# Performance work log

Measured on AMD Instinct MI355X. Metric: run time of the kernel, lower is better.

The kernel has to match this reference:

```python
import jax, jax.numpy as jnp
import numpy as np

NUM_HEADS = 8
CODEBOOK_SIZE = 1024
HEAD_DIM = 128
BATCH = 32768


def setup_inputs() -> dict:
    key = jax.random.key(0)
    k_z, k_cb = jax.random.split(key)
    z = jax.random.normal(k_z, (BATCH, NUM_HEADS * HEAD_DIM), dtype=jnp.float32)
    codebooks = jax.random.normal(k_cb, (NUM_HEADS, CODEBOOK_SIZE, HEAD_DIM), dtype=jnp.float32)
    return {"z": z, "codebooks": codebooks}


def reference(z, codebooks):
    # z: [B, H*D]; codebooks: [H, K, D]
    H, K, D = codebooks.shape
    B = z.shape[0]
    zh = z.reshape(B, H, D)
    # Squared euclidean distances ||z - c||^2 = ||z||^2 - 2 z.c + ||c||^2.
    # torch.cdist(p=2) applies sqrt, but sqrt is monotone so argmin is identical.
    z_sq = jnp.sum(zh * zh, axis=-1)                       # [B, H]
    c_sq = jnp.sum(codebooks * codebooks, axis=-1)         # [H, K]
    cross = jnp.einsum('bhd,hkd->bhk', zh, codebooks)      # [B, H, K]
    d2 = z_sq[:, :, None] - 2.0 * cross + c_sq[None, :, :]  # [B, H, K]
    idx = jnp.argmin(d2, axis=-1)                          # [B, H] int
    # Gather nearest codes per head: codebooks[h, idx[b,h]] -> [B, H, D]
    zq = codebooks[jnp.arange(H)[None, :], idx]
    # Straight-through estimator: forward = codes, backward = identity on z.
    zq = zh + jax.lax.stop_gradient(zq - zh)
    return zq.reshape(B, H * D), idx
```

## Files before the change

kernel.cpp:

```cpp
#include <hip/hip_runtime.h>

namespace {
constexpr int kNH = 8;
constexpr int kK  = 1024;
constexpr int kD  = 128;
constexpr int kB  = 32768;

constexpr int BM  = 128;
constexpr int kMarginQ = 4;
constexpr float kMarginF32 = 0.0625f;

constexpr size_t kOffCsq = 4096;
constexpr size_t kOffCbF = 65536;
constexpr size_t kOffWl  = 65536 + 2 * 2097152;
}

typedef short bf16x8 __attribute__((ext_vector_type(8)));
typedef float f32x16 __attribute__((ext_vector_type(16)));

__device__ __forceinline__ unsigned short f2bf_rne(float f) {
    unsigned int x = __float_as_uint(f);
    unsigned int r = (x + 0x7fffu + ((x >> 16) & 1u)) >> 16;
    return (unsigned short)r;
}
__device__ __forceinline__ float bf2f(unsigned short u) {
    return __uint_as_float(((unsigned int)u) << 16);
}

__global__ void pq_prep(const float* __restrict__ cb,
                        unsigned short* __restrict__ cbf,
                        float* __restrict__ csq)
{
    int code = blockIdx.x;
    int t = threadIdx.x;
    int h = code >> 10, k = code & 1023;
    int kt = k >> 6, cv = (k >> 5) & 1, l31 = k & 31;
    int kc = t >> 4, hh = (t >> 3) & 1, j = t & 7;
    float v = cb[(size_t)code * kD + t];
    unsigned short hb = f2bf_rne(v);
    unsigned short lb = f2bf_rne(v - bf2f(hb));
    size_t base = ((((size_t)h * 16 + kt) * 8 + kc) * 2 + cv) * 2048;
    size_t off  = base + (hh * 32 + l31) * 16 + j * 2;
    *(unsigned short*)((char*)cbf + off)        = hb;
    *(unsigned short*)((char*)cbf + off + 1024) = lb;
    __shared__ double red[128];
    red[t] = (double)v * (double)v;
    __syncthreads();
    for (int s = 64; s > 0; s >>= 1) {
        if (t < s) red[t] += red[t + s];
        __syncthreads();
    }
    if (t == 0) csq[code] = (float)(red[0] * 1024.0);
}

__global__ __launch_bounds__(256, 2)
void pq_coarse_mfma3(const float* __restrict__ z, const float* __restrict__ cb,
                     const unsigned short* __restrict__ cbf,
                     const float* __restrict__ csq1024,
                     float* __restrict__ out_zq, float* __restrict__ out_idx,
                     unsigned int* wl_count, unsigned int* wl, unsigned int wl_cap)
{
    __shared__ float csq_s[kK];
    __shared__ int   idx_s[BM];

    const int t    = threadIdx.x;
    const int h    = blockIdx.y;
    const int b0   = blockIdx.x * BM;
    const int lane = t & 63;
    const int w    = t >> 6;
    const int l31  = lane & 31, h32 = lane >> 5;

    *(float4*)&csq_s[t * 4] = *(const float4*)(csq1024 + h * kK + t * 4);

    bf16x8 Ah[8], Al[8];
    {
        const float* zr = z + (size_t)(b0 + w * 32 + l31) * (kNH * kD) + h * kD + h32 * 8;
        #pragma unroll
        for (int kc = 0; kc < 8; ++kc) {
            float4 a = *(const float4*)(zr + kc * 16);
            float4 b = *(const float4*)(zr + kc * 16 + 4);
            float f[8] = {a.x, a.y, a.z, a.w, b.x, b.y, b.z, b.w};
            bf16x8 hv, lv;
            #pragma unroll
            for (int j = 0; j < 8; ++j) {
                unsigned short hb = f2bf_rne(f[j]);
                hv[j] = (short)hb;
                lv[j] = (short)f2bf_rne(f[j] - bf2f(hb));
            }
            Ah[kc] = hv;
            Al[kc] = lv;
        }
    }
    __syncthreads();

    int b1[16], b2[16];
    #pragma unroll
    for (int r = 0; r < 16; ++r) { b1[r] = 0x7fffffff; b2[r] = 0x7fffffff; }

    const char* bbase = (const char*)cbf + (size_t)h * 524288 + lane * 16;
#define LDSLOT(kt_, kc_, s_)                                                  \
    {                                                                         \
        const char* p_ = bbase + (size_t)(((kt_) * 8 + (kc_)) * 2) * 2048;    \
        Bh0[s_] = *(const bf16x8*)(p_);                                       \
        Bl0[s_] = *(const bf16x8*)(p_ + 1024);                                \
        Bh1[s_] = *(const bf16x8*)(p_ + 2048);                                \
        Bl1[s_] = *(const bf16x8*)(p_ + 3072);                                \
    }

    bf16x8 Bh0[4], Bl0[4], Bh1[4], Bl1[4];
    LDSLOT(0, 0, 0);
    LDSLOT(0, 1, 1);

    for (int kt = 0; kt < 16; ++kt) {
        f32x16 acc0 = (f32x16)0.0f, acc1 = (f32x16)0.0f;
        const int ktn = (kt + 1 < 16) ? kt + 1 : kt;
        #pragma unroll
        for (int kc = 0; kc < 8; ++kc) {
            const int s  = kc & 3;
            const int s2 = (kc + 2) & 3;
            if (kc < 6) {
                LDSLOT(kt, kc + 2, s2);
            } else {
                LDSLOT(ktn, kc - 6, s2);
            }
            __builtin_amdgcn_s_setprio(1);
            acc0 = __builtin_amdgcn_mfma_f32_32x32x16_bf16(Ah[kc], Bh0[s], acc0, 0, 0, 0);
            acc1 = __builtin_amdgcn_mfma_f32_32x32x16_bf16(Ah[kc], Bh1[s], acc1, 0, 0, 0);
            acc0 = __builtin_amdgcn_mfma_f32_32x32x16_bf16(Al[kc], Bh0[s], acc0, 0, 0, 0);
            acc1 = __builtin_amdgcn_mfma_f32_32x32x16_bf16(Al[kc], Bh1[s], acc1, 0, 0, 0);
            acc0 = __builtin_amdgcn_mfma_f32_32x32x16_bf16(Ah[kc], Bl0[s], acc0, 0, 0, 0);
            acc1 = __builtin_amdgcn_mfma_f32_32x32x16_bf16(Ah[kc], Bl1[s], acc1, 0, 0, 0);
            __builtin_amdgcn_s_setprio(0);
        }
        const float cs0 = csq_s[kt * 64 + l31];
        const float cs1 = csq_s[kt * 64 + 32 + l31];
        const int   kg0 = kt * 64 + l31, kg1 = kg0 + 32;
        #pragma unroll
        for (int r = 0; r < 16; ++r) {
            {
                float kf = fmaf(acc0[r], -2048.0f, cs0);
                int key = ((int)kf << 10) + kg0;
                int mx = max(b1[r], key);
                b1[r] = min(b1[r], key);
                b2[r] = min(b2[r], mx);
            }
            {
                float kf = fmaf(acc1[r], -2048.0f, cs1);
                int key = ((int)kf << 10) + kg1;
                int mx = max(b1[r], key);
                b1[r] = min(b1[r], key);
                b2[r] = min(b2[r], mx);
            }
        }
    }
#undef LDSLOT

    #pragma unroll
    for (int r = 0; r < 16; ++r) {
        int v1 = b1[r], v2 = b2[r];
        #pragma unroll
        for (int m = 1; m < 32; m <<= 1) {
            int o1 = __shfl_xor(v1, m);
            int o2 = __shfl_xor(v2, m);
            int mx = max(v1, o1);
            v1 = min(v1, o1);
            v2 = min(min(v2, o2), mx);
        }
        if (l31 == 0) {
            int row = w * 32 + (r & 3) + ((r >> 2) << 3) + h32 * 4;
            int idx = v1 & 1023;
            idx_s[row] = idx;
            int gid = (b0 + row) * kNH + h;
            out_idx[gid] = (float)idx;
            if (wl_cap > 0u && ((v2 >> 10) - (v1 >> 10)) <= kMarginQ) {
                unsigned int pos = atomicAdd(wl_count, 1u);
                if (pos < wl_cap) wl[pos] = (unsigned int)gid;
            }
        }
    }
    __syncthreads();
    {
        const float* cbh_row = cb + (size_t)h * kK * kD;
        #pragma unroll
        for (int it = 0; it < 16; ++it) {
            int c = it * 256 + t;
            int row = c >> 5, col4 = c & 31;
            *(float4*)(out_zq + (size_t)(b0 + row) * (kNH * kD) + h * kD + col4 * 4) =
                *(const float4*)(cbh_row + (size_t)idx_s[row] * kD + col4 * 4);
        }
    }
}

__global__ __launch_bounds__(256, 2)
void pq_coarse_f32(const float* __restrict__ z, const float* __restrict__ cb,
                   float* __restrict__ out_zq, float* __restrict__ out_idx,
                   unsigned int* wl_count, unsigned int* wl, unsigned int wl_cap)
{
    constexpr int KT = 64, PAD = 68, BMF = 64;
    __shared__ float zT[kD][PAD];
    __shared__ float cT[kD][PAD];
    __shared__ float csq_s[KT];
    __shared__ int   bidx_s[BMF];

    const int t  = threadIdx.x;
    const int h  = blockIdx.y;
    const int b0 = blockIdx.x * BMF;
    const int tx = t & 15, ty = t >> 4;
    const int r8 = t & 7,  d4 = t >> 3;

    {
        const float* zp = z + (size_t)(b0 + r8) * (kNH * kD) + h * kD + 4 * d4;
        #pragma unroll
        for (int it = 0; it < BMF / 8; ++it) {
            float4 v = *(const float4*)(zp + (size_t)(8 * it) * (kNH * kD));
            int r = r8 + 8 * it;
            zT[4 * d4 + 0][r] = v.x; zT[4 * d4 + 1][r] = v.y;
            zT[4 * d4 + 2][r] = v.z; zT[4 * d4 + 3][r] = v.w;
        }
    }
    float best1[4], best2[4]; int ibest[4];
    #pragma unroll
    for (int i = 0; i < 4; ++i) { best1[i] = 3.4e38f; best2[i] = 3.4e38f; ibest[i] = 0; }

    for (int kt = 0; kt < kK / KT; ++kt) {
        __syncthreads();
        {
            const float* cp = cb + ((size_t)h * kK + kt * KT + r8) * kD + 4 * d4;
            #pragma unroll
            for (int it = 0; it < KT / 8; ++it) {
                float4 v = *(const float4*)(cp + (size_t)(8 * it) * kD);
                int r = r8 + 8 * it;
                cT[4 * d4 + 0][r] = v.x; cT[4 * d4 + 1][r] = v.y;
                cT[4 * d4 + 2][r] = v.z; cT[4 * d4 + 3][r] = v.w;
            }
        }
        if (t < KT) csq_s[t] = 0.0f;
        __syncthreads();
        {
            int kk = t & 63, part = t >> 6;
            float s = 0.f;
            #pragma unroll
            for (int i = 0; i < 32; ++i) { float v = cT[32 * part + i][kk]; s = fmaf(v, v, s); }
            atomicAdd(&csq_s[kk], s);
        }
        __syncthreads();
        float accA[4][4] = {{0}}, accB[4][4] = {{0}};
        #pragma unroll 2
        for (int d = 0; d < kD; d += 2) {
            float4 za = *(const float4*)&zT[d][4 * ty];
            float4 ca = *(const float4*)&cT[d][4 * tx];
            float4 zb = *(const float4*)&zT[d + 1][4 * ty];
            float4 cv = *(const float4*)&cT[d + 1][4 * tx];
            float zav[4] = {za.x, za.y, za.z, za.w}, cav[4] = {ca.x, ca.y, ca.z, ca.w};
            float zbv[4] = {zb.x, zb.y, zb.z, zb.w}, cbv[4] = {cv.x, cv.y, cv.z, cv.w};
            #pragma unroll
            for (int i = 0; i < 4; ++i)
                #pragma unroll
                for (int j = 0; j < 4; ++j) {
                    accA[i][j] = fmaf(zav[i], cav[j], accA[i][j]);
                    accB[i][j] = fmaf(zbv[i], cbv[j], accB[i][j]);
                }
        }
        #pragma unroll
        for (int j = 0; j < 4; ++j) {
            int kk = 4 * tx + j;
            float cs = csq_s[kk];
            int kg = kt * KT + kk;
            #pragma unroll
            for (int i = 0; i < 4; ++i) {
                float s = fmaf(-2.0f, accA[i][j] + accB[i][j], cs);
                if (s < best1[i]) { best2[i] = best1[i]; best1[i] = s; ibest[i] = kg; }
                else if (s < best2[i]) { best2[i] = s; }
            }
        }
    }
    __syncthreads();
    float* redv1 = &zT[0][0];
    float* redv2 = redv1 + BMF * 16;
    int*   redi  = (int*)(redv2 + BMF * 16);
    #pragma unroll
    for (int i = 0; i < 4; ++i) {
        int r = 4 * ty + i;
        redv1[r * 16 + tx] = best1[i]; redv2[r * 16 + tx] = best2[i]; redi[r * 16 + tx] = ibest[i];
    }
    __syncthreads();
    if (t < BMF) {
        int r = t;
        float vb1_ = redv1[r * 16], vb2_ = redv2[r * 16];
        int i1 = redi[r * 16];
        #pragma unroll
        for (int x = 1; x < 16; ++x) {
            float nb1 = redv1[r * 16 + x], nb2 = redv2[r * 16 + x];
            int ni1 = redi[r * 16 + x];
            if (nb1 < vb1_ || (nb1 == vb1_ && ni1 < i1)) { vb2_ = fminf(vb1_, nb2); vb1_ = nb1; i1 = ni1; }
            else vb2_ = fminf(vb2_, nb1);
        }
        bidx_s[r] = i1;
        int gid = (b0 + r) * kNH + h;
        out_idx[gid] = (float)i1;
        if (wl_cap > 0u && (vb2_ - vb1_) <= kMarginF32) {
            unsigned int pos = atomicAdd(wl_count, 1u);
            if (pos < wl_cap) wl[pos] = (unsigned int)gid;
        }
    }
    __syncthreads();
    {
        int r = t >> 2, q = t & 3;
        const float* src = cb + ((size_t)h * kK + bidx_s[r]) * kD;
        float* dst = out_zq + (size_t)(b0 + r) * (kNH * kD) + h * kD;
        #pragma unroll
        for (int m = 0; m < 8; ++m) {
            int jj = 4 * m + q;
            *(float4*)(dst + 4 * jj) = *(const float4*)(src + 4 * jj);
        }
    }
}

__global__ __launch_bounds__(256)
void pq_exact(const float* __restrict__ z, const float* __restrict__ cb,
              float* __restrict__ out_zq, float* __restrict__ out_idx,
              const unsigned int* wl_count, const unsigned int* wl,
              unsigned int wl_cap)
{
    if (wl_cap == 0u) return;
    __shared__ float  zs[kD];
    __shared__ double rv[256];
    __shared__ int    ri[256];
    unsigned int n = *wl_count;
    if (n > wl_cap) n = wl_cap;
    const int t = threadIdx.x;
    for (unsigned int e = blockIdx.x; e < n; e += gridDim.x) {
        unsigned int id = wl[e];
        int b = (int)(id / kNH), h = (int)(id % kNH);
        if (t < kD) zs[t] = z[(size_t)b * (kNH * kD) + h * kD + t];
        __syncthreads();
        double bv = 1e300; int bi = 0;
        #pragma unroll
        for (int kk = 0; kk < 4; ++kk) {
            int k = t * 4 + kk;
            const float* c = cb + ((size_t)h * kK + k) * kD;
            double s = 0.0;
            for (int d = 0; d < kD; ++d) {
                double diff = (double)zs[d] - (double)c[d];
                s = fma(diff, diff, s);
            }
            if (s < bv) { bv = s; bi = k; }
        }
        rv[t] = bv; ri[t] = bi;
        __syncthreads();
        for (int s2 = 128; s2 > 0; s2 >>= 1) {
            if (t < s2) {
                if (rv[t + s2] < rv[t] || (rv[t + s2] == rv[t] && ri[t + s2] < ri[t])) {
                    rv[t] = rv[t + s2]; ri[t] = ri[t + s2];
                }
            }
            __syncthreads();
        }
        int kbest = ri[0];
        if (t == 0) out_idx[id] = (float)kbest;
        if (t < kD)
            out_zq[(size_t)b * (kNH * kD) + h * kD + t] =
                cb[((size_t)h * kK + kbest) * kD + t];
        __syncthreads();
    }
}

extern "C" void kernel_launch(void* const* d_in, const int* in_sizes, int n_in,
                              void* d_out, int out_size, void* d_ws, size_t ws_size,
                              hipStream_t stream)
{
    const float* z  = (const float*)d_in[0];
    const float* cb = (const float*)d_in[1];
    float* out_zq  = (float*)d_out;
    float* out_idx = out_zq + (size_t)kB * kNH * kD;
    char* ws = (char*)d_ws;

    if (ws_size >= kOffWl + 4096) {
        unsigned int* wl_count = (unsigned int*)ws;
        unsigned int* wl = (unsigned int*)(ws + kOffWl);
        size_t c = (ws_size - kOffWl) / 4;
        unsigned int cap = (unsigned int)(c > 262144 ? 262144 : c);
        float* csq = (float*)(ws + kOffCsq);
        unsigned short* cbf = (unsigned short*)(ws + kOffCbF);

        hipMemsetAsync(d_ws, 0, 4, stream);
        pq_prep<<<kNH * kK, kD, 0, stream>>>(cb, cbf, csq);
        dim3 grid(kB / BM, kNH);
        pq_coarse_mfma3<<<grid, 256, 0, stream>>>(z, cb, cbf, csq,
                                                  out_zq, out_idx, wl_count, wl, cap);
        pq_exact<<<256, 256, 0, stream>>>(z, cb, out_zq, out_idx, wl_count, wl, cap);
    } else {
        unsigned int* wl_count = (unsigned int*)ws;
        unsigned int* wl = wl_count + 1;
        unsigned int cap = 0;
        if (ws_size >= 64) {
            size_t c = ws_size / 4 - 1;
            cap = (unsigned int)(c > 262144 ? 262144 : c);
            hipMemsetAsync(d_ws, 0, 4, stream);
        }
        dim3 grid(kB / 64, kNH);
        pq_coarse_f32<<<grid, 256, 0, stream>>>(z, cb, out_zq, out_idx, wl_count, wl, cap);
        pq_exact<<<256, 256, 0, stream>>>(z, cb, out_zq, out_idx, wl_count, wl, cap);
    }
}
```

Measured before the change: 252.9 us.

## Keep codebook slices in registers and stream z tiles through LDS

Adds a new coarse kernel that keeps each wave's 64-code slice of the split-bf16 codebook resident in registers. It streams 32-row tiles of z through double-buffered, swizzled LDS, converting z to hi/lo bf16 on the fly. Work is split across two codebook halves. Each block writes per-row top-2 partial keys to a workspace, and a new merge kernel combines the halves, writes indices and gathered codes, and builds the refinement worklist. This trades the old per-block codebook streaming for codebook reuse across many z rows. The cost is an extra kernel launch, a partial-result buffer round trip, and a larger workspace requirement that falls back to the old path when unavailable.

Measured after the change: 238.4 us. 5.7% less time.

```diff
diff --git a/kernel.cpp b/kernel.cpp
--- a/kernel.cpp
+++ b/kernel.cpp
@@ -10,13 +10,16 @@
 constexpr int kMarginQ = 4;
 constexpr float kMarginF32 = 0.0625f;
 
-constexpr size_t kOffCsq = 4096;
-constexpr size_t kOffCbF = 65536;
-constexpr size_t kOffWl  = 65536 + 2 * 2097152;
-}
-
-typedef short bf16x8 __attribute__((ext_vector_type(8)));
-typedef float f32x16 __attribute__((ext_vector_type(16)));
+constexpr size_t kOffCsq  = 4096;
+constexpr size_t kOffCbF  = 65536;
+constexpr size_t kOffPart = 65536 + 4194304;
+constexpr size_t kOffWl6  = 65536 + 8388608;
+constexpr size_t kOffWl5  = 65536 + 4194304;
+}
+
+typedef short           bf16x8 __attribute__((ext_vector_type(8)));
+typedef unsigned short  us16x8 __attribute__((ext_vector_type(8)));
+typedef float           f32x16 __attribute__((ext_vector_type(16)));
 
 __device__ __forceinline__ unsigned short f2bf_rne(float f) {
     unsigned int x = __float_as_uint(f);
@@ -53,6 +56,173 @@
     if (t == 0) csq[code] = (float)(red[0] * 1024.0);
 }
 
+__global__ __launch_bounds__(512, 2)
+void pq_coarse_mfma4(const float* __restrict__ z,
+                     const unsigned short* __restrict__ cbf,
+                     const float* __restrict__ csq1024,
+                     int2* __restrict__ part)
+{
+    __shared__ unsigned short zbuf[2][2][32 * kD];
+    __shared__ int2 P[2][8][32];
+
+    const int t    = threadIdx.x;
+    const int lane = t & 63;
+    const int w    = t >> 6;
+    const int l31  = lane & 31, h32 = lane >> 5;
+    const int h    = blockIdx.y;
+    const int half = blockIdx.z;
+    const int rb0  = blockIdx.x * 1024;
+
+    bf16x8 Ah[8][2], Al[8][2];
+    {
+        const char* base = (const char*)cbf
+            + (((size_t)h * 16 + half * 8 + w) * 16) * 2048 + lane * 16;
+        #pragma unroll
+        for (int kc = 0; kc < 8; ++kc)
+            #pragma unroll
+            for (int cv = 0; cv < 2; ++cv) {
+                const char* p = base + (size_t)(kc * 2 + cv) * 2048;
+                Ah[kc][cv] = *(const bf16x8*)p;
+                Al[kc][cv] = *(const bf16x8*)(p + 1024);
+            }
+    }
+    float csel[2][16];
+    {
+        const float* cs = csq1024 + h * kK + half * 512 + w * 64 + h32 * 4;
+        #pragma unroll
+        for (int cv = 0; cv < 2; ++cv)
+            #pragma unroll
+            for (int r = 0; r < 16; ++r)
+                csel[cv][r] = cs[cv * 32 + (r & 3) + ((r >> 2) << 3)];
+    }
+
+    float4 zA, zB;
+    auto issueZ = [&](int tile) {
+        const float* zp = z + (size_t)(rb0 + tile * 32 + (t >> 4)) * (kNH * kD)
+                            + h * kD + (t & 15) * 8;
+        zA = *(const float4*)zp;
+        zB = *(const float4*)(zp + 4);
+    };
+    auto commitZ = [&](int buf) {
+        float f[8] = {zA.x, zA.y, zA.z, zA.w, zB.x, zB.y, zB.z, zB.w};
+        us16x8 hv, lv;
+        #pragma unroll
+        for (int j = 0; j < 8; ++j) {
+            unsigned short hb = f2bf_rne(f[j]);
+            hv[j] = hb;
+            lv[j] = f2bf_rne(f[j] - bf2f(hb));
+        }
+        int r = t >> 4, seg = t & 15;
+        int off = r * 256 + ((seg * 16) ^ ((r & 15) << 4));
+        *(us16x8*)((char*)&zbuf[buf][0][0] + off) = hv;
+        *(us16x8*)((char*)&zbuf[buf][1][0] + off) = lv;
+    };
+    auto mergeP = [&](int pb, int tile) {
+        int2 m = P[pb][0][t];
+        int m1 = m.x, m2 = m.y;
+        #pragma unroll
+        for (int ww = 1; ww < 8; ++ww) {
+            int2 p = P[pb][ww][t];
+            int mx = max(m1, p.x);
+            m1 = min(m1, p.x);
+            m2 = min(min(m2, p.y), mx);
+        }
+        int gid = (rb0 + tile * 32 + t) * kNH + h;
+        part[(size_t)gid * 2 + half] = make_int2(m1, m2);
+    };
+
+    issueZ(0);
+    commitZ(0);
+    __syncthreads();
+
+    int cur = 0;
+    const int cgb = half * 512 + w * 64 + h32 * 4;
+    for (int tile = 0; tile < 32; ++tile) {
+        if (tile + 1 < 32) issueZ(tile + 1);
+        if (tile > 0 && t < 32) mergeP(cur ^ 1, tile - 1);
+
+        f32x16 acc0 = (f32x16)0.0f, acc1 = (f32x16)0.0f;
+        const char* zh0 = (const char*)&zbuf[cur][0][0];
+        const char* zl0 = (const char*)&zbuf[cur][1][0];
+        const int boff = l31 * 256;
+        const int swz  = (l31 & 15) << 4;
+        #pragma unroll
+        for (int kc = 0; kc < 8; ++kc) {
+            int col = (kc * 32 + h32 * 16) ^ swz;
+            bf16x8 Bh = *(const bf16x8*)(zh0 + boff + col);
+            bf16x8 Bl = *(const bf16x8*)(zl0 + boff + col);
+            __builtin_amdgcn_s_setprio(1);
+            acc0 = __builtin_amdgcn_mfma_f32_32x32x16_bf16(Ah[kc][0], Bh, acc0, 0, 0, 0);
+            acc1 = __builtin_amdgcn_mfma_f32_32x32x16_bf16(Ah[kc][1], Bh, acc1, 0, 0, 0);
+            acc0 = __builtin_amdgcn_mfma_f32_32x32x16_bf16(Al[kc][0], Bh, acc0, 0, 0, 0);
+            acc1 = __builtin_amdgcn_mfma_f32_32x32x16_bf16(Al[kc][1], Bh, acc1, 0, 0, 0);
+            acc0 = __builtin_amdgcn_mfma_f32_32x32x16_bf16(Ah[kc][0], Bl, acc0, 0, 0, 0);
+            acc1 = __builtin_amdgcn_mfma_f32_32x32x16_bf16(Ah[kc][1], Bl, acc1, 0, 0, 0);
+            __builtin_amdgcn_s_setprio(0);
+        }
+        int b1 = 0x7fffffff, b2 = 0x7fffffff;
+        #pragma unroll
+        for (int r = 0; r < 16; ++r) {
+            int cr = (r & 3) + ((r >> 2) << 3);
+            {
+                float kf = fmaf(acc0[r], -2048.0f, csel[0][r]);
+                int key = ((int)kf << 10) + cgb + cr;
+                int mx = max(b1, key); b1 = min(b1, key); b2 = min(b2, mx);
+            }
+            {
+                float kf = fmaf(acc1[r], -2048.0f, csel[1][r]);
+                int key = ((int)kf << 10) + cgb + cr + 32;
+                int mx = max(b1, key); b1 = min(b1, key); b2 = min(b2, mx);
+            }
+        }
+        int o1 = __shfl_xor(b1, 32), o2 = __shfl_xor(b2, 32);
+        int mx2 = max(b1, o1);
+        int v1 = min(b1, o1);
+        int v2 = min(min(b2, o2), mx2);
+        if (h32 == 0) P[cur][w][l31] = make_int2(v1, v2);
+
+        if (tile + 1 < 32) commitZ(cur ^ 1);
+        __syncthreads();
+        cur ^= 1;
+    }
+    if (t < 32) mergeP(cur ^ 1, 31);
+}
+
+__global__ __launch_bounds__(256)
+void pq_merge(const int2* __restrict__ part, const float* __restrict__ cb,
+              float* __restrict__ out_zq, float* __restrict__ out_idx,
+              unsigned int* wl_count, unsigned int* wl, unsigned int wl_cap)
+{
+    __shared__ int idx_s[128];
+    const int t = threadIdx.x;
+    const int g0 = blockIdx.x * 128;
+    if (t < 128) {
+        int gid = g0 + t;
+        int2 p0 = part[(size_t)gid * 2];
+        int2 p1 = part[(size_t)gid * 2 + 1];
+        int mx = max(p0.x, p1.x);
+        int v1 = min(p0.x, p1.x);
+        int v2 = min(min(p0.y, p1.y), mx);
+        int idx = v1 & 1023;
+        idx_s[t] = idx;
+        out_idx[gid] = (float)idx;
+        if (wl_cap > 0u && ((v2 >> 10) - (v1 >> 10)) <= kMarginQ) {
+            unsigned int pos = atomicAdd(wl_count, 1u);
+            if (pos < wl_cap) wl[pos] = (unsigned int)gid;
+        }
+    }
+    __syncthreads();
+    #pragma unroll
+    for (int it = 0; it < 16; ++it) {
+        int c = it * 256 + t;
+        int row = c >> 5, c4 = c & 31;
+        int gid = g0 + row;
+        int b = gid >> 3, hh = gid & 7;
+        *(float4*)(out_zq + (size_t)b * (kNH * kD) + hh * kD + c4 * 4) =
+            *(const float4*)(cb + ((size_t)hh * kK + idx_s[row]) * kD + c4 * 4);
+    }
+}
+
 __global__ __launch_bounds__(256, 2)
 void pq_coarse_mfma3(const float* __restrict__ z, const float* __restrict__ cb,
                      const unsigned short* __restrict__ cbf,
@@ -118,11 +288,7 @@
         for (int kc = 0; kc < 8; ++kc) {
             const int s  = kc & 3;
             const int s2 = (kc + 2) & 3;
-            if (kc < 6) {
-                LDSLOT(kt, kc + 2, s2);
-            } else {
-                LDSLOT(ktn, kc - 6, s2);
-            }
+            if (kc < 6) { LDSLOT(kt, kc + 2, s2); } else { LDSLOT(ktn, kc - 6, s2); }
             __builtin_amdgcn_s_setprio(1);
             acc0 = __builtin_amdgcn_mfma_f32_32x32x16_bf16(Ah[kc], Bh0[s], acc0, 0, 0, 0);
             acc1 = __builtin_amdgcn_mfma_f32_32x32x16_bf16(Ah[kc], Bh1[s], acc1, 0, 0, 0);
@@ -140,16 +306,12 @@
             {
                 float kf = fmaf(acc0[r], -2048.0f, cs0);
                 int key = ((int)kf << 10) + kg0;
-                int mx = max(b1[r], key);
-                b1[r] = min(b1[r], key);
-                b2[r] = min(b2[r], mx);
+                int mx = max(b1[r], key); b1[r] = min(b1[r], key); b2[r] = min(b2[r], mx);
             }
             {
                 float kf = fmaf(acc1[r], -2048.0f, cs1);
                 int key = ((int)kf << 10) + kg1;
-                int mx = max(b1[r], key);
-                b1[r] = min(b1[r], key);
-                b2[r] = min(b2[r], mx);
+                int mx = max(b1[r], key); b1[r] = min(b1[r], key); b2[r] = min(b2[r], mx);
             }
         }
     }
@@ -375,10 +537,26 @@
     float* out_idx = out_zq + (size_t)kB * kNH * kD;
     char* ws = (char*)d_ws;
 
-    if (ws_size >= kOffWl + 4096) {
+    if (ws_size >= kOffWl6 + 65536) {
         unsigned int* wl_count = (unsigned int*)ws;
-        unsigned int* wl = (unsigned int*)(ws + kOffWl);
-        size_t c = (ws_size - kOffWl) / 4;
+        unsigned int* wl = (unsigned int*)(ws + kOffWl6);
+        size_t c = (ws_size - kOffWl6) / 4;
+        unsigned int cap = (unsigned int)(c > 262144 ? 262144 : c);
+        float* csq = (float*)(ws + kOffCsq);
+        unsigned short* cbf = (unsigned short*)(ws + kOffCbF);
+        int2* part = (int2*)(ws + kOffPart);
+
+        hipMemsetAsync(d_ws, 0, 4, stream);
+        pq_prep<<<kNH * kK, kD, 0, stream>>>(cb, cbf, csq);
+        dim3 grid(32, kNH, 2);
+        pq_coarse_mfma4<<<grid, 512, 0, stream>>>(z, cbf, csq, part);
+        pq_merge<<<kB * kNH / 128, 256, 0, stream>>>(part, cb, out_zq, out_idx,
+                                                     wl_count, wl, cap);
+        pq_exact<<<256, 256, 0, stream>>>(z, cb, out_zq, out_idx, wl_count, wl, cap);
+    } else if (ws_size >= kOffWl5 + 4096) {
+        unsigned int* wl_count = (unsigned int*)ws;
+        unsigned int* wl = (unsigned int*)(ws + kOffWl5);
+        size_t c = (ws_size - kOffWl5) / 4;
         unsigned int cap = (unsigned int)(c > 262144 ? 262144 : c);
         float* csq = (float*)(ws + kOffCsq);
         unsigned short* cbf = (unsigned short*)(ws + kOffCbF);
```
